# Kernel tuning notes

Measured on AMD Instinct MI355X. Metric: run time of the kernel, lower is better.

## Reference

```python
import jax, jax.numpy as jnp
import numpy as np
import itertools

N_PARTICLES = 8388608
GRID_RES = 2048
BOX_SIZE = 1000.0

def _rotations_47():
    perms = list(itertools.permutations([0, 1, 2]))
    signs = list(itertools.product([1, -1], repeat=3))
    mats = []
    for s in signs:
        for p in perms:
            M = np.zeros((3, 3), np.float32)
            M[0, p[0]] = s[0]; M[1, p[1]] = s[1]; M[2, p[2]] = s[2]
            mats.append(M)
    return jnp.asarray(np.stack(mats)[1:])  # drop identity -> 47 matrices

# Analytic stand-ins for jax_cosmo background quantities (EdS-like forms).
def _Gp(a):
    return a ** 1.5

def _dGfa(a):
    return 1.5 * jnp.sqrt(a)

def _a_of_chi(chi):
    return 1.0 / (1.0 + chi / 3000.0)

def _paint_2d(pos, center, width, box_size, res):
    """CIC scatter of particles inside a z-slab onto a [res,res] density plane."""
    z = pos[:, 2]
    sel = ((z >= center - width * 0.5) & (z < center + width * 0.5)).astype(pos.dtype)
    xy = pos[:, :2] * (res / box_size)          # grid coordinates, [N,2]
    i0 = jnp.floor(xy)
    f = xy - i0                                  # CIC fractional offsets
    i0 = i0.astype(jnp.int32)
    ix0 = jnp.mod(i0[:, 0], res); iy0 = jnp.mod(i0[:, 1], res)
    ix1 = jnp.mod(i0[:, 0] + 1, res); iy1 = jnp.mod(i0[:, 1] + 1, res)
    fx, fy = f[:, 0], f[:, 1]
    flat = jnp.zeros((res * res,), dtype=pos.dtype)
    flat = flat.at[ix0 * res + iy0].add(sel * (1 - fx) * (1 - fy))
    flat = flat.at[ix1 * res + iy0].add(sel * fx * (1 - fy))
    flat = flat.at[ix0 * res + iy1].add(sel * (1 - fx) * fy)
    flat = flat.at[ix1 * res + iy1].add(sel * fx * fy)
    return flat.reshape(res, res)

def setup_inputs():
    key = jax.random.key(0)
    k1, k2 = jax.random.split(key)
    positions = jax.random.uniform(k1, (N_PARTICLES, 3), jnp.float32) * BOX_SIZE
    velocities = jax.random.normal(k2, (N_PARTICLES, 3), jnp.float32) * 2.0
    return {
        "positions": positions,
        "velocities": velocities,
        "rotations": _rotations_47(),
        "observer": jnp.zeros((3,), jnp.float32),
        "r_centers": jnp.asarray([250.0, 750.0, 1250.0, 1750.0], jnp.float32),
        "density_widths": jnp.full((4,), 500.0, jnp.float32),
        "t": jnp.float32(0.8),
        "max_comoving_distance": jnp.float32(BOX_SIZE),
        "box_size": jnp.float32(BOX_SIZE),
        "shell_idx": 2,
        "rotation_idx": 1,
        "grid_res": GRID_RES,
    }

def reference(positions, velocities, rotations, observer, r_centers, density_widths,
              t, max_comoving_distance, box_size, shell_idx, rotation_idx, grid_res):
    r_center = r_centers[shell_idx]
    width = density_widths[shell_idx]
    inside_box = r_center + width * 0.5 <= max_comoving_distance

    def inside_branch(args):
        pos, _vel = args
        return _paint_2d(pos, r_center, width, box_size, grid_res)

    def telephoto_branch(args):
        pos, vel = args
        M = rotations[rotation_idx % 47]                                   # [3,3]
        shift = jnp.floor(r_center / max_comoving_distance) * max_comoving_distance
        p_rot = (pos - observer) @ M.T                                      # rotate about observer
        z_axis = jnp.array([0.0, 0.0, 1.0], pos.dtype)
        p_shift = p_rot + z_axis * shift
        v_rot = vel @ M.T
        dist = jnp.linalg.norm(p_shift - observer, axis=-1)                 # [N]
        a_tgt = _a_of_chi(dist)[:, None]                                    # per-particle target scale factor
        ac = jnp.sqrt(t * a_tgt)
        drift = (_Gp(a_tgt) - _Gp(t)) / _dGfa(ac)
        p_drift = p_shift + drift * v_rot
        return _paint_2d(p_drift + observer, r_center, width, box_size, grid_res)

    return jax.lax.cond(inside_box, inside_branch, telephoto_branch, (positions, velocities))
```

## Files before the change

kernel.cpp:

```cpp
#include <hip/hip_runtime.h>
#include <cmath>


#define TSZ    128
#define NBKT   256
#define NXCC   8
#define CAP    4096
#define DEPTH  32
#define NTH    256
#define NBLK   1024
#define DESCMAX 512

__device__ __forceinline__ int get_xcc_id() {
    int x = __builtin_amdgcn_s_getreg((3 << 11) | (0 << 6) | 20);
    return x & (NXCC - 1);
}

__device__ __forceinline__ int wrap_idx(int v, int res) {
    v += (v < 0) ? res : 0;
    v += (v < 0) ? res : 0;
    v += (v < 0) ? res : 0;
    v -= (v >= res) ? res : 0;
    v -= (v >= res) ? res : 0;
    v -= (v >= res) ? res : 0;
    if (v < 0 || v >= res) { v %= res; if (v < 0) v += res; }
    return v;
}

__device__ __forceinline__ void scatter_direct(float* __restrict__ out, int res,
                                               int gx0, int gy0, float fx, float fy) {
    int gx1 = gx0 + 1; if (gx1 >= res) gx1 = 0;
    int gy1 = gy0 + 1; if (gy1 >= res) gy1 = 0;
    atomicAdd(&out[gx0 * res + gy0], (1.0f - fx) * (1.0f - fy));
    atomicAdd(&out[gx1 * res + gy0], fx * (1.0f - fy));
    atomicAdd(&out[gx0 * res + gy1], (1.0f - fx) * fy);
    atomicAdd(&out[gx1 * res + gy1], fx * fy);
}

__device__ __forceinline__ void rec_decode(unsigned rec, int b, int tiles,
                                           int& gx, int& gy, float& fx, float& fy) {
    int tx = b / tiles, ty = b - tx * tiles;
    gx = (tx << 7) + (int)(rec >> 25);
    gy = (ty << 7) + (int)((rec >> 18) & 127u);
    fx = (float)((rec >> 9) & 511u) * (1.0f / 512.0f);
    fy = (float)(rec & 511u) * (1.0f / 512.0f);
}

__device__ __forceinline__ bool transform_particle(
    const float* __restrict__ pos, const float* __restrict__ vel,
    const float* __restrict__ rotations, const float* __restrict__ observer,
    float r_center, float width, float maxd, float t, bool inside, int ridx,
    int i, float& X, float& Y)
{
    float px = pos[3 * i + 0];
    float py = pos[3 * i + 1];
    float pz = pos[3 * i + 2];

    float Z;
    if (inside) {
        X = px; Y = py; Z = pz;
    } else {
        const float* M = rotations + 9 * ridx;
        const float ox = observer[0], oy = observer[1], oz = observer[2];

        const float qx = px - ox, qy = py - oy, qz = pz - oz;
        float rx = M[0] * qx + M[1] * qy + M[2] * qz;
        float ry = M[3] * qx + M[4] * qy + M[5] * qz;
        float rz = M[6] * qx + M[7] * qy + M[8] * qz;

        const float shift = floorf(r_center / maxd) * maxd;
        rz += shift;

        const float vx = vel[3 * i + 0];
        const float vy = vel[3 * i + 1];
        const float vz = vel[3 * i + 2];
        const float vrx = M[0] * vx + M[1] * vy + M[2] * vz;
        const float vry = M[3] * vx + M[4] * vy + M[5] * vz;
        const float vrz = M[6] * vx + M[7] * vy + M[8] * vz;

        const float dx = rx - ox, dy = ry - oy, dz = rz - oz;
        const float dist  = sqrtf(dx * dx + dy * dy + dz * dz);
        const float a_tgt = 1.0f / (1.0f + dist / 3000.0f);
        const float ac    = sqrtf(t * a_tgt);
        const float gp_a  = a_tgt * sqrtf(a_tgt);
        const float gp_t  = t * sqrtf(t);
        const float drift = (gp_a - gp_t) / (1.5f * sqrtf(ac));

        X = rx + drift * vrx + ox;
        Y = ry + drift * vry + oy;
        Z = rz + drift * vrz + oz;
    }
    return (Z >= r_center - width * 0.5f) && (Z < r_center + width * 0.5f);
}

__global__ __launch_bounds__(NTH) void tp_bin(
    const float* __restrict__ pos, const float* __restrict__ vel,
    const float* __restrict__ rotations, const float* __restrict__ observer,
    const float* __restrict__ r_centers, const float* __restrict__ widths,
    const float* __restrict__ t_p, const float* __restrict__ maxd_p,
    const float* __restrict__ box_p, const int* __restrict__ shell_p,
    const int* __restrict__ ridx_p,
    unsigned* __restrict__ gcnt, unsigned* __restrict__ grec,
    float* __restrict__ out, int res, int tiles, int n, int rounds)
{
    __shared__ unsigned fill[NBKT];
    __shared__ unsigned buf[NBKT * DEPTH];
    __shared__ unsigned descB[DESCMAX];
    __shared__ unsigned descD[DESCMAX];
    __shared__ unsigned ndesc;

    const int tid = threadIdx.x;
    for (int b = tid; b < NBKT; b += NTH) fill[b] = 0;
    if (tid == 0) ndesc = 0;

    const int   shell    = shell_p[0];
    const float r_center = r_centers[shell];
    const float width    = widths[shell];
    const float maxd     = maxd_p[0];
    const float box      = box_p[0];
    const float t        = t_p[0];
    const bool  inside   = (r_center + width * 0.5f) <= maxd;
    int ridx = ridx_p[0] % 47; if (ridx < 0) ridx += 47;

    const int xcc = get_xcc_id();
    const int segbase = xcc * NBKT;
    const float scale = (float)res / box;

    __syncthreads();

    for (int r = 0; r < rounds; ++r) {
        const int i = (r * NBLK + blockIdx.x) * NTH + tid;
        bool valid = (i < n);
        unsigned rec = 0; int st = 0, ix0 = 0, iy0 = 0;
        float fx = 0.f, fy = 0.f;
        if (valid) {
            float X, Y;
            valid = transform_particle(pos, vel, rotations, observer, r_center,
                                       width, maxd, t, inside, ridx, i, X, Y);
            if (valid) {
                const float gx = X * scale, gy = Y * scale;
                const float fgx = floorf(gx), fgy = floorf(gy);
                fx = gx - fgx; fy = gy - fgy;
                ix0 = wrap_idx((int)fgx, res);
                iy0 = wrap_idx((int)fgy, res);
                st = (ix0 >> 7) * tiles + (iy0 >> 7);
                unsigned qx = (unsigned)(fx * 512.0f + 0.5f); if (qx > 511u) qx = 511u;
                unsigned qy = (unsigned)(fy * 512.0f + 0.5f); if (qy > 511u) qy = 511u;
                rec = ((unsigned)(ix0 & 127) << 25) | ((unsigned)(iy0 & 127) << 18)
                    | (qx << 9) | qy;
            }
        }
        if (valid) {
            unsigned p = atomicAdd(&fill[st], 1u);
            if (p < DEPTH) buf[st * DEPTH + p] = rec;
            else { atomicSub(&fill[st], 1u); scatter_direct(out, res, ix0, iy0, fx, fy); }
        }
        __syncthreads();
        if (tid < NBKT) {
            const unsigned c = fill[tid];
            const unsigned k = c >> 4;
            if (k) {
                unsigned gbase = atomicAdd(&gcnt[segbase + tid], 16u * k);
                unsigned d = atomicAdd(&ndesc, k);
                for (unsigned g = 0; g < k; ++g) {
                    descB[d + g] = (unsigned)tid | ((g * 16u) << 16);
                    descD[d + g] = gbase + 16u * g;
                }
            }
        }
        __syncthreads();
        const unsigned nd = ndesc;
        for (unsigned did = (unsigned)(tid >> 4); did < nd; did += NTH / 16) {
            const unsigned e = descB[did];
            const unsigned b = e & 0xffffu, so = e >> 16;
            const unsigned dst = descD[did] + (unsigned)(tid & 15);
            const unsigned rv = buf[b * DEPTH + so + (tid & 15)];
            if (dst < CAP) {
                grec[(size_t)(segbase + b) * CAP + dst] = rv;
            } else {
                int gx0, gy0; float ffx, ffy;
                rec_decode(rv, (int)b, tiles, gx0, gy0, ffx, ffy);
                scatter_direct(out, res, gx0, gy0, ffx, ffy);
            }
        }
        __syncthreads();
        if (tid < NBKT) {
            const unsigned c = fill[tid];
            const unsigned k = c >> 4;
            if (k) {
                const unsigned resid = c - 16u * k;
                for (unsigned j = 0; j < resid; ++j)
                    buf[tid * DEPTH + j] = buf[tid * DEPTH + 16u * k + j];
                fill[tid] = resid;
            }
        }
        if (tid == 0) ndesc = 0;
        __syncthreads();
    }

    if (tid < NBKT) {
        const unsigned c = fill[tid];
        if (c) {
            unsigned d = atomicAdd(&ndesc, 1u);
            unsigned gbase = atomicAdd(&gcnt[segbase + tid], c);
            descB[d] = (unsigned)tid | (c << 16);
            descD[d] = gbase;
        }
    }
    __syncthreads();
    const unsigned nd = ndesc;
    for (unsigned did = (unsigned)(tid >> 4); did < nd; did += NTH / 16) {
        const unsigned e = descB[did];
        const unsigned b = e & 0xffffu, c = e >> 16;
        const unsigned lane = (unsigned)(tid & 15);
        if (lane < c) {
            const unsigned dst = descD[did] + lane;
            const unsigned rv = buf[b * DEPTH + lane];
            if (dst < CAP) {
                grec[(size_t)(segbase + b) * CAP + dst] = rv;
            } else {
                int gx0, gy0; float ffx, ffy;
                rec_decode(rv, (int)b, tiles, gx0, gy0, ffx, ffy);
                scatter_direct(out, res, gx0, gy0, ffx, ffy);
            }
        }
    }
}

__global__ __launch_bounds__(1024) void tp_paint(
    const unsigned* __restrict__ gcnt, const unsigned* __restrict__ grec,
    float* __restrict__ out, int res, int tiles)
{
    __shared__ unsigned long long quad[4][64 * 64];
    const int b = blockIdx.x;
    const int tx = b / tiles, ty = b - tx * tiles;

    for (int c = threadIdx.x; c < 4 * 64 * 64; c += blockDim.x)
        quad[c >> 12][c & 4095] = 0ull;
    __syncthreads();

    for (int x = 0; x < NXCC; ++x) {
        unsigned m = gcnt[x * NBKT + b]; if (m > CAP) m = CAP;
        const unsigned* rr = grec + (size_t)(x * NBKT + b) * CAP;
        for (unsigned k = threadIdx.x; k < m; k += blockDim.x) {
            const unsigned p = rr[k];
            const int li = (int)(p >> 25);
            const int lj = (int)((p >> 18) & 127u);
            const unsigned qx = (p >> 9) & 511u;
            const unsigned qy = p & 511u;
            const unsigned ax = 512u - qx, ay = 512u - qy;
            const unsigned long long w00 = (ax * ay + 128u) >> 8;
            const unsigned long long w01 = (ax * qy + 128u) >> 8;
            const unsigned long long w10 = (qx * ay + 128u) >> 8;
            const unsigned long long w11 = (qx * qy + 128u) >> 8;
            const unsigned long long pk = w00 | (w01 << 16) | (w10 << 32) | (w11 << 48);
            const int g = ((li & 1) << 1) | (lj & 1);
            atomicAdd(&quad[g][(li >> 1) * 64 + (lj >> 1)], pk);
        }
    }
    __syncthreads();

    for (int c = threadIdx.x; c < (TSZ + 1) * (TSZ + 1); c += blockDim.x) {
        const int i = c / (TSZ + 1), j = c - i * (TSZ + 1);
        unsigned acc = 0;
        #pragma unroll
        for (int r = 0; r < 2; ++r) {
            const int ii = i - r;
            if (ii < 0 || ii > TSZ - 1) continue;
            #pragma unroll
            for (int s = 0; s < 2; ++s) {
                const int jj = j - s;
                if (jj < 0 || jj > TSZ - 1) continue;
                const int g = ((ii & 1) << 1) | (jj & 1);
                const unsigned long long v = quad[g][(ii >> 1) * 64 + (jj >> 1)];
                acc += (unsigned)((v >> (16 * (r * 2 + s))) & 0xffffull);
            }
        }
        const float val = (float)acc * (1.0f / 1024.0f);
        int gx = tx * TSZ + i; if (gx >= res) gx -= res;
        int gy = ty * TSZ + j; if (gy >= res) gy -= res;
        float* dst = &out[gx * res + gy];
        if (i == 0 || j == 0 || i == TSZ || j == TSZ) {
            if (val != 0.0f) atomicAdd(dst, val);
        } else {
            *dst += val;
        }
    }
}

__global__ __launch_bounds__(256) void tp_direct(
    const float* __restrict__ pos, const float* __restrict__ vel,
    const float* __restrict__ rotations, const float* __restrict__ observer,
    const float* __restrict__ r_centers, const float* __restrict__ widths,
    const float* __restrict__ t_p, const float* __restrict__ maxd_p,
    const float* __restrict__ box_p, const int* __restrict__ shell_p,
    const int* __restrict__ ridx_p, float* __restrict__ out, int res, int n)
{
    int i = blockIdx.x * blockDim.x + threadIdx.x;
    if (i >= n) return;
    const int   shell    = shell_p[0];
    const float r_center = r_centers[shell];
    const float width    = widths[shell];
    const float maxd     = maxd_p[0];
    const float box      = box_p[0];
    const float t        = t_p[0];
    const bool  inside   = (r_center + width * 0.5f) <= maxd;
    int ridx = ridx_p[0] % 47; if (ridx < 0) ridx += 47;

    float X, Y;
    if (!transform_particle(pos, vel, rotations, observer, r_center, width,
                            maxd, t, inside, ridx, i, X, Y))
        return;

    const float scale = (float)res / box;
    const float gx = X * scale, gy = Y * scale;
    const float fgx = floorf(gx), fgy = floorf(gy);
    scatter_direct(out, res, wrap_idx((int)fgx, res), wrap_idx((int)fgy, res),
                   gx - fgx, gy - fgy);
}

extern "C" void kernel_launch(void* const* d_in, const int* in_sizes, int n_in,
                              void* d_out, int out_size, void* d_ws, size_t ws_size,
                              hipStream_t stream) {
    const float* pos   = (const float*)d_in[0];
    const float* velv  = (const float*)d_in[1];
    const float* rot   = (const float*)d_in[2];
    const float* obs   = (const float*)d_in[3];
    const float* rc    = (const float*)d_in[4];
    const float* dw    = (const float*)d_in[5];
    const float* t     = (const float*)d_in[6];
    const float* maxd  = (const float*)d_in[7];
    const float* box   = (const float*)d_in[8];
    const int*   shell = (const int*)d_in[9];
    const int*   ridx  = (const int*)d_in[10];
    float* out = (float*)d_out;

    const int n   = in_sizes[0] / 3;
    const int res = (int)llround(sqrt((double)out_size));

    hipMemsetAsync(out, 0, (size_t)out_size * sizeof(float), stream);

    const int tiles = res / TSZ;
    const int nt2 = tiles * tiles;
    const size_t cnt_bytes = (size_t)NXCC * NBKT * sizeof(unsigned);
    const size_t rec_bytes = (size_t)NXCC * NBKT * CAP * sizeof(unsigned);

    if (res % TSZ != 0 || nt2 > NBKT ||
        (long long)res * res != (long long)out_size ||
        ws_size < cnt_bytes + rec_bytes) {
        tp_direct<<<(n + 255) / 256, 256, 0, stream>>>(
            pos, velv, rot, obs, rc, dw, t, maxd, box, shell, ridx, out, res, n);
        return;
    }

    unsigned* gcnt = (unsigned*)d_ws;
    unsigned* grec = (unsigned*)((char*)d_ws + cnt_bytes);

    hipMemsetAsync(gcnt, 0, cnt_bytes, stream);

    const int rounds = (n + NBLK * NTH - 1) / (NBLK * NTH);
    tp_bin<<<NBLK, NTH, 0, stream>>>(
        pos, velv, rot, obs, rc, dw, t, maxd, box, shell, ridx,
        gcnt, grec, out, res, tiles, n, rounds);

    tp_paint<<<nt2, 1024, 0, stream>>>(gcnt, grec, out, res, tiles);
}
```

Baseline: 291.0 us.

## Process four particles per thread with float4 loads and hoisted uniforms

The binning kernel now handles four particles per thread in each round. It reads positions and velocities as three float4 loads each, so the number of rounds and the block-wide synchronisation and flush steps they carry drop by a factor of four. Uniform parameters (rotation matrix, observer, slab bounds, gp(t)) are computed once per block. The sqrt and divide calls in the drift maths are replaced with hardware rcp/sqrt intrinsics, and the modulo wrap becomes a power-of-two mask, with a fallback to the direct path when the resolution is not a power of two. The risks are slightly lower precision in the drift maths and higher register pressure from the unrolled per-thread work.

```diff
diff --git a/kernel.cpp b/kernel.cpp
--- a/kernel.cpp
+++ b/kernel.cpp
@@ -9,12 +9,16 @@
 #define DEPTH  32
 #define NTH    256
 #define NBLK   1024
+#define VEC    4
 #define DESCMAX 512
 
 __device__ __forceinline__ int get_xcc_id() {
     int x = __builtin_amdgcn_s_getreg((3 << 11) | (0 << 6) | 20);
     return x & (NXCC - 1);
 }
+
+__device__ __forceinline__ float fast_rcp(float x)  { return __builtin_amdgcn_rcpf(x); }
+__device__ __forceinline__ float fast_sqrt(float x) { return __builtin_amdgcn_sqrtf(x); }
 
 __device__ __forceinline__ int wrap_idx(int v, int res) {
     v += (v < 0) ? res : 0;
@@ -46,51 +50,60 @@
     fy = (float)(rec & 511u) * (1.0f / 512.0f);
 }
 
-__device__ __forceinline__ bool transform_particle(
-    const float* __restrict__ pos, const float* __restrict__ vel,
-    const float* __restrict__ rotations, const float* __restrict__ observer,
-    float r_center, float width, float maxd, float t, bool inside, int ridx,
-    int i, float& X, float& Y)
+struct Uni {
+    float m00, m01, m02, m10, m11, m12, m20, m21, m22;
+    float ox, oy, oz, shift;
+    float r_lo, r_hi, t, gp_t, scale;
+    int   resm1, res, tiles;
+    bool  inside;
+};
+
+__device__ __forceinline__ void tp_process(
+    const Uni& u, float px, float py, float pz, float vx, float vy, float vz,
+    unsigned* __restrict__ fill, unsigned* __restrict__ buf,
+    float* __restrict__ out)
 {
-    float px = pos[3 * i + 0];
-    float py = pos[3 * i + 1];
-    float pz = pos[3 * i + 2];
-
-    float Z;
-    if (inside) {
+    float X, Y, Z;
+    if (u.inside) {
         X = px; Y = py; Z = pz;
     } else {
-        const float* M = rotations + 9 * ridx;
-        const float ox = observer[0], oy = observer[1], oz = observer[2];
-
-        const float qx = px - ox, qy = py - oy, qz = pz - oz;
-        float rx = M[0] * qx + M[1] * qy + M[2] * qz;
-        float ry = M[3] * qx + M[4] * qy + M[5] * qz;
-        float rz = M[6] * qx + M[7] * qy + M[8] * qz;
-
-        const float shift = floorf(r_center / maxd) * maxd;
-        rz += shift;
-
-        const float vx = vel[3 * i + 0];
-        const float vy = vel[3 * i + 1];
-        const float vz = vel[3 * i + 2];
-        const float vrx = M[0] * vx + M[1] * vy + M[2] * vz;
-        const float vry = M[3] * vx + M[4] * vy + M[5] * vz;
-        const float vrz = M[6] * vx + M[7] * vy + M[8] * vz;
-
-        const float dx = rx - ox, dy = ry - oy, dz = rz - oz;
-        const float dist  = sqrtf(dx * dx + dy * dy + dz * dz);
-        const float a_tgt = 1.0f / (1.0f + dist / 3000.0f);
-        const float ac    = sqrtf(t * a_tgt);
-        const float gp_a  = a_tgt * sqrtf(a_tgt);
-        const float gp_t  = t * sqrtf(t);
-        const float drift = (gp_a - gp_t) / (1.5f * sqrtf(ac));
-
-        X = rx + drift * vrx + ox;
-        Y = ry + drift * vry + oy;
-        Z = rz + drift * vrz + oz;
-    }
-    return (Z >= r_center - width * 0.5f) && (Z < r_center + width * 0.5f);
+        const float qx_ = px - u.ox, qy_ = py - u.oy, qz_ = pz - u.oz;
+        float rx = u.m00 * qx_ + u.m01 * qy_ + u.m02 * qz_;
+        float ry = u.m10 * qx_ + u.m11 * qy_ + u.m12 * qz_;
+        float rz = u.m20 * qx_ + u.m21 * qy_ + u.m22 * qz_ + u.shift;
+
+        const float vrx = u.m00 * vx + u.m01 * vy + u.m02 * vz;
+        const float vry = u.m10 * vx + u.m11 * vy + u.m12 * vz;
+        const float vrz = u.m20 * vx + u.m21 * vy + u.m22 * vz;
+
+        const float dx = rx - u.ox, dy = ry - u.oy, dz = rz - u.oz;
+        const float dist  = fast_sqrt(dx * dx + dy * dy + dz * dz);
+        const float a_tgt = fast_rcp(1.0f + dist * (1.0f / 3000.0f));
+        const float ac    = fast_sqrt(u.t * a_tgt);
+        const float gp_a  = a_tgt * fast_sqrt(a_tgt);
+        const float drift = (gp_a - u.gp_t) * fast_rcp(1.5f * fast_sqrt(ac));
+
+        X = rx + drift * vrx + u.ox;
+        Y = ry + drift * vry + u.oy;
+        Z = rz + drift * vrz + u.oz;
+    }
+    if (!(Z >= u.r_lo && Z < u.r_hi)) return;
+
+    const float gx = X * u.scale, gy = Y * u.scale;
+    const float fgx = floorf(gx), fgy = floorf(gy);
+    const float fx = gx - fgx, fy = gy - fgy;
+    const int ix0 = ((int)fgx) & u.resm1;
+    const int iy0 = ((int)fgy) & u.resm1;
+    const int st = (ix0 >> 7) * u.tiles + (iy0 >> 7);
+
+    unsigned qx = (unsigned)(fx * 512.0f + 0.5f); if (qx > 511u) qx = 511u;
+    unsigned qy = (unsigned)(fy * 512.0f + 0.5f); if (qy > 511u) qy = 511u;
+    const unsigned rec = ((unsigned)(ix0 & 127) << 25) | ((unsigned)(iy0 & 127) << 18)
+                       | (qx << 9) | qy;
+
+    unsigned p = atomicAdd(&fill[st], 1u);
+    if (p < DEPTH) buf[st * DEPTH + p] = rec;
+    else { atomicSub(&fill[st], 1u); scatter_direct(out, u.res, ix0, iy0, fx, fy); }
 }
 
 __global__ __launch_bounds__(NTH) void tp_bin(
@@ -113,47 +126,63 @@
     for (int b = tid; b < NBKT; b += NTH) fill[b] = 0;
     if (tid == 0) ndesc = 0;
 
-    const int   shell    = shell_p[0];
-    const float r_center = r_centers[shell];
-    const float width    = widths[shell];
-    const float maxd     = maxd_p[0];
-    const float box      = box_p[0];
-    const float t        = t_p[0];
-    const bool  inside   = (r_center + width * 0.5f) <= maxd;
-    int ridx = ridx_p[0] % 47; if (ridx < 0) ridx += 47;
+    Uni u;
+    {
+        const int   shell    = shell_p[0];
+        const float r_center = r_centers[shell];
+        const float width    = widths[shell];
+        const float maxd     = maxd_p[0];
+        const float box      = box_p[0];
+        u.t      = t_p[0];
+        u.inside = (r_center + width * 0.5f) <= maxd;
+        int ridx = ridx_p[0] % 47; if (ridx < 0) ridx += 47;
+        const float* M = rotations + 9 * ridx;
+        u.m00 = M[0]; u.m01 = M[1]; u.m02 = M[2];
+        u.m10 = M[3]; u.m11 = M[4]; u.m12 = M[5];
+        u.m20 = M[6]; u.m21 = M[7]; u.m22 = M[8];
+        u.ox = observer[0]; u.oy = observer[1]; u.oz = observer[2];
+        u.shift = floorf(r_center / maxd) * maxd;
+        u.r_lo = r_center - width * 0.5f;
+        u.r_hi = r_center + width * 0.5f;
+        u.gp_t = u.t * sqrtf(u.t);
+        u.scale = (float)res / box;
+        u.resm1 = res - 1; u.res = res; u.tiles = tiles;
+    }
 
     const int xcc = get_xcc_id();
     const int segbase = xcc * NBKT;
-    const float scale = (float)res / box;
+    const float4* __restrict__ pos4 = (const float4*)pos;
+    const float4* __restrict__ vel4 = (const float4*)vel;
 
     __syncthreads();
 
     for (int r = 0; r < rounds; ++r) {
-        const int i = (r * NBLK + blockIdx.x) * NTH + tid;
-        bool valid = (i < n);
-        unsigned rec = 0; int st = 0, ix0 = 0, iy0 = 0;
-        float fx = 0.f, fy = 0.f;
-        if (valid) {
-            float X, Y;
-            valid = transform_particle(pos, vel, rotations, observer, r_center,
-                                       width, maxd, t, inside, ridx, i, X, Y);
-            if (valid) {
-                const float gx = X * scale, gy = Y * scale;
-                const float fgx = floorf(gx), fgy = floorf(gy);
-                fx = gx - fgx; fy = gy - fgy;
-                ix0 = wrap_idx((int)fgx, res);
-                iy0 = wrap_idx((int)fgy, res);
-                st = (ix0 >> 7) * tiles + (iy0 >> 7);
-                unsigned qx = (unsigned)(fx * 512.0f + 0.5f); if (qx > 511u) qx = 511u;
-                unsigned qy = (unsigned)(fy * 512.0f + 0.5f); if (qy > 511u) qy = 511u;
-                rec = ((unsigned)(ix0 & 127) << 25) | ((unsigned)(iy0 & 127) << 18)
-                    | (qx << 9) | qy;
-            }
-        }
-        if (valid) {
-            unsigned p = atomicAdd(&fill[st], 1u);
-            if (p < DEPTH) buf[st * DEPTH + p] = rec;
-            else { atomicSub(&fill[st], 1u); scatter_direct(out, res, ix0, iy0, fx, fy); }
+        const int base = ((r * NBLK + blockIdx.x) * NTH + tid) * VEC;
+        if (base + VEC <= n) {
+            const int q = base * 3 / 4;
+            const float4 a = pos4[q], b = pos4[q + 1], c = pos4[q + 2];
+            if (u.inside) {
+                float4 z; z.x = 0; z.y = 0; z.z = 0; z.w = 0;
+                tp_process(u, a.x, a.y, a.z, 0, 0, 0, fill, buf, out);
+                tp_process(u, a.w, b.x, b.y, 0, 0, 0, fill, buf, out);
+                tp_process(u, b.z, b.w, c.x, 0, 0, 0, fill, buf, out);
+                tp_process(u, c.y, c.z, c.w, 0, 0, 0, fill, buf, out);
+                (void)z;
+            } else {
+                const float4 d = vel4[q], e = vel4[q + 1], f = vel4[q + 2];
+                tp_process(u, a.x, a.y, a.z, d.x, d.y, d.z, fill, buf, out);
+                tp_process(u, a.w, b.x, b.y, d.w, e.x, e.y, fill, buf, out);
+                tp_process(u, b.z, b.w, c.x, e.z, e.w, f.x, fill, buf, out);
+                tp_process(u, c.y, c.z, c.w, f.y, f.z, f.w, fill, buf, out);
+            }
+        } else {
+            for (int p = 0; p < VEC; ++p) {
+                const int i = base + p;
+                if (i < n)
+                    tp_process(u, pos[3 * i], pos[3 * i + 1], pos[3 * i + 2],
+                               vel[3 * i], vel[3 * i + 1], vel[3 * i + 2],
+                               fill, buf, out);
+            }
         }
         __syncthreads();
         if (tid < NBKT) {
@@ -179,8 +208,8 @@
                 grec[(size_t)(segbase + b) * CAP + dst] = rv;
             } else {
                 int gx0, gy0; float ffx, ffy;
-                rec_decode(rv, (int)b, tiles, gx0, gy0, ffx, ffy);
-                scatter_direct(out, res, gx0, gy0, ffx, ffy);
+                rec_decode(rv, (int)b, u.tiles, gx0, gy0, ffx, ffy);
+                scatter_direct(out, u.res, gx0, gy0, ffx, ffy);
             }
         }
         __syncthreads();
@@ -220,8 +249,8 @@
                 grec[(size_t)(segbase + b) * CAP + dst] = rv;
             } else {
                 int gx0, gy0; float ffx, ffy;
-                rec_decode(rv, (int)b, tiles, gx0, gy0, ffx, ffy);
-                scatter_direct(out, res, gx0, gy0, ffx, ffy);
+                rec_decode(rv, (int)b, u.tiles, gx0, gy0, ffx, ffy);
+                scatter_direct(out, u.res, gx0, gy0, ffx, ffy);
             }
         }
     }
@@ -307,10 +336,31 @@
     const bool  inside   = (r_center + width * 0.5f) <= maxd;
     int ridx = ridx_p[0] % 47; if (ridx < 0) ridx += 47;
 
-    float X, Y;
-    if (!transform_particle(pos, vel, rotations, observer, r_center, width,
-                            maxd, t, inside, ridx, i, X, Y))
-        return;
+    float px = pos[3 * i], py = pos[3 * i + 1], pz = pos[3 * i + 2];
+    float X, Y, Z;
+    if (inside) {
+        X = px; Y = py; Z = pz;
+    } else {
+        const float* M = rotations + 9 * ridx;
+        const float ox = observer[0], oy = observer[1], oz = observer[2];
+        const float qx = px - ox, qy = py - oy, qz = pz - oz;
+        float rx = M[0] * qx + M[1] * qy + M[2] * qz;
+        float ry = M[3] * qx + M[4] * qy + M[5] * qz;
+        float rz = M[6] * qx + M[7] * qy + M[8] * qz + floorf(r_center / maxd) * maxd;
+        const float vx = vel[3 * i], vy = vel[3 * i + 1], vz = vel[3 * i + 2];
+        const float vrx = M[0] * vx + M[1] * vy + M[2] * vz;
+        const float vry = M[3] * vx + M[4] * vy + M[5] * vz;
+        const float vrz = M[6] * vx + M[7] * vy + M[8] * vz;
+        const float dx = rx - ox, dy = ry - oy, dz = rz - oz;
+        const float dist  = sqrtf(dx * dx + dy * dy + dz * dz);
+        const float a_tgt = 1.0f / (1.0f + dist / 3000.0f);
+        const float ac    = sqrtf(t * a_tgt);
+        const float drift = (a_tgt * sqrtf(a_tgt) - t * sqrtf(t)) / (1.5f * sqrtf(ac));
+        X = rx + drift * vrx + ox;
+        Y = ry + drift * vry + oy;
+        Z = rz + drift * vrz + oz;
+    }
+    if (!(Z >= r_center - width * 0.5f && Z < r_center + width * 0.5f)) return;
 
     const float scale = (float)res / box;
     const float gx = X * scale, gy = Y * scale;
@@ -344,8 +394,9 @@
     const int nt2 = tiles * tiles;
     const size_t cnt_bytes = (size_t)NXCC * NBKT * sizeof(unsigned);
     const size_t rec_bytes = (size_t)NXCC * NBKT * CAP * sizeof(unsigned);
-
-    if (res % TSZ != 0 || nt2 > NBKT ||
+    const bool pow2 = res > 0 && (res & (res - 1)) == 0;
+
+    if (!pow2 || res % TSZ != 0 || nt2 > NBKT ||
         (long long)res * res != (long long)out_size ||
         ws_size < cnt_bytes + rec_bytes) {
         tp_direct<<<(n + 255) / 256, 256, 0, stream>>>(
@@ -358,7 +409,8 @@
 
     hipMemsetAsync(gcnt, 0, cnt_bytes, stream);
 
-    const int rounds = (n + NBLK * NTH - 1) / (NBLK * NTH);
+    const int per_round = NBLK * NTH * VEC;
+    const int rounds = (n + per_round - 1) / per_round;
     tp_bin<<<NBLK, NTH, 0, stream>>>(
         pos, velv, rot, obs, rc, dw, t, maxd, box, shell, ridx,
         gcnt, grec, out, res, tiles, n, rounds);
```

Measured after the change: 282.4 us. -3.0%, faster.
